# Optimization experiments

Measured on AMD Instinct MI355X. Metric: run time of the kernel, lower is better.

The kernel has to match this reference:

```python
import jax, jax.numpy as jnp
import numpy as np

B, T, C, H = 2, 2048, 2048, 16
HS = C // H
EPS = 1e-5


def _ln(x, w, b):
    mu = jnp.mean(x, axis=-1, keepdims=True)
    var = jnp.mean(jnp.square(x - mu), axis=-1, keepdims=True)
    return (x - mu) * jax.lax.rsqrt(var + EPS) * w + b


def setup_inputs() -> dict:
    key = jax.random.key(0)
    ks = jax.random.split(key, 8)
    s = 0.02
    return {
        "x": jax.random.normal(ks[0], (B, T, C), jnp.float32),
        "ln1_w": jnp.ones((C,), jnp.float32),
        "ln1_b": jnp.zeros((C,), jnp.float32),
        "w_qkv": jax.random.normal(ks[1], (C, 3 * C), jnp.float32) * s,
        "b_qkv": jnp.zeros((3 * C,), jnp.float32),
        "w_proj": jax.random.normal(ks[2], (C, C), jnp.float32) * s,
        "b_proj": jnp.zeros((C,), jnp.float32),
        "ln2_w": jnp.ones((C,), jnp.float32),
        "ln2_b": jnp.zeros((C,), jnp.float32),
        "w_fc": jax.random.normal(ks[3], (C, 4 * C), jnp.float32) * s,
        "b_fc": jnp.zeros((4 * C,), jnp.float32),
        "w_fc2": jax.random.normal(ks[4], (4 * C, C), jnp.float32) * s,
        "b_fc2": jnp.zeros((C,), jnp.float32),
    }


def reference(x, ln1_w, ln1_b, w_qkv, b_qkv, w_proj, b_proj,
              ln2_w, ln2_b, w_fc, b_fc, w_fc2, b_fc2):
    # --- attention branch (kv_cache=None -> L=0, burst=False, no padding mask) ---
    h = _ln(x, ln1_w, ln1_b)
    qkv = h @ w_qkv + b_qkv  # (B, T, 3C)
    q, k, v = jnp.split(qkv, 3, axis=-1)
    q = q.reshape(B, T, H, HS).transpose(0, 2, 1, 3)  # (B, H, T, HS)
    k = k.reshape(B, T, H, HS).transpose(0, 2, 1, 3)
    v = v.reshape(B, T, H, HS).transpose(0, 2, 1, 3)
    att = jnp.einsum('bhqd,bhkd->bhqk', q, k) * (1.0 / np.sqrt(HS))
    causal = jnp.tril(jnp.ones((T, T), bool))  # bias[0:T, 0:T]
    att = jnp.where(causal, att, -jnp.inf)
    att = jax.nn.softmax(att, axis=-1)
    y = jnp.einsum('bhqk,bhkd->bhqd', att, v)
    y = y.transpose(0, 2, 1, 3).reshape(B, T, C)
    y = y @ w_proj + b_proj
    x = x + y
    # --- MLP branch ---
    h = _ln(x, ln2_w, ln2_b)
    h = jax.nn.gelu(h @ w_fc + b_fc, approximate=False)
    x = x + (h @ w_fc2 + b_fc2)
    return x
```

## Files before the change

### kernel.cpp

```cpp
#include <hip/hip_runtime.h>
#include <hip/hip_bf16.h>
#include <cstdint>
#include <cstddef>

typedef __attribute__((ext_vector_type(8))) short bf16x8;
typedef __attribute__((ext_vector_type(4))) float f32x4;

#define DEVI __device__ __forceinline__

DEVI unsigned short f2bf(float f) {
  union { float f; unsigned u; } x; x.f = f;
  unsigned r = x.u + 0x7fffu + ((x.u >> 16) & 1u);
  return (unsigned short)(r >> 16);
}

DEVI float exp2fast(float x) {
#if __has_builtin(__builtin_amdgcn_exp2f)
  return __builtin_amdgcn_exp2f(x);
#else
  return exp2f(x);
#endif
}

DEVI void gload_lds16(const void* g, void* l) {
  __builtin_amdgcn_global_load_lds((const __attribute__((address_space(1))) void*)g,
                                   (__attribute__((address_space(3))) void*)l, 16, 0, 0);
}

DEVI f32x4 mfma16(bf16x8 a, bf16x8 b, f32x4 c) {
  return __builtin_amdgcn_mfma_f32_16x16x32_bf16(a, b, c, 0, 0, 0);
}

__global__ __launch_bounds__(256) void transpose_to_bf16(
    const float* __restrict__ w, unsigned short* __restrict__ wt, int K, int N) {
  __shared__ float tile[32][33];
  const int n0 = blockIdx.x * 32, k0 = blockIdx.y * 32;
  const int tx = threadIdx.x, ty = threadIdx.y;
#pragma unroll
  for (int i = 0; i < 4; i++)
    tile[ty + i * 8][tx] = w[(size_t)(k0 + ty + i * 8) * N + n0 + tx];
  __syncthreads();
#pragma unroll
  for (int i = 0; i < 4; i++)
    wt[(size_t)(n0 + ty + i * 8) * K + k0 + tx] = f2bf(tile[tx][ty + i * 8]);
}

__global__ __launch_bounds__(256) void transpose_v(
    const unsigned short* __restrict__ in, unsigned short* __restrict__ out) {
  __shared__ unsigned short tile[32][33];
  const int bh = blockIdx.z;
  const unsigned short* inp = in + (size_t)bh * 2048 * 128;
  unsigned short* op = out + (size_t)bh * 2048 * 128;
  const int t0 = blockIdx.x * 32, d0 = blockIdx.y * 32;
  const int tx = threadIdx.x, ty = threadIdx.y;
#pragma unroll
  for (int i = 0; i < 4; i++)
    tile[ty + i * 8][tx] = inp[(size_t)(t0 + ty + i * 8) * 128 + d0 + tx];
  __syncthreads();
#pragma unroll
  for (int i = 0; i < 4; i++)
    op[(size_t)(d0 + ty + i * 8) * 2048 + t0 + tx] = tile[tx][ty + i * 8];
}

__global__ __launch_bounds__(256) void ln_kernel(
    const float* __restrict__ x, const float* __restrict__ gw,
    const float* __restrict__ gb, unsigned short* __restrict__ out) {
  __shared__ float red[8];
  const int row = blockIdx.x, tid = threadIdx.x;
  const float* xr = x + (size_t)row * 2048;
  f32x4 a = *((const f32x4*)xr + tid * 2);
  f32x4 b = *((const f32x4*)xr + tid * 2 + 1);
  float s = a[0] + a[1] + a[2] + a[3] + b[0] + b[1] + b[2] + b[3];
#pragma unroll
  for (int m = 32; m >= 1; m >>= 1) s += __shfl_xor(s, m, 64);
  if ((tid & 63) == 0) red[tid >> 6] = s;
  __syncthreads();
  const float mu = (red[0] + red[1] + red[2] + red[3]) * (1.f / 2048.f);
  float d[8]; float ss = 0.f;
#pragma unroll
  for (int j = 0; j < 8; j++) {
    float v = ((j < 4) ? a[j] : b[j - 4]) - mu;
    d[j] = v; ss += v * v;
  }
#pragma unroll
  for (int m = 32; m >= 1; m >>= 1) ss += __shfl_xor(ss, m, 64);
  __syncthreads();
  if ((tid & 63) == 0) red[4 + (tid >> 6)] = ss;
  __syncthreads();
  const float var = (red[4] + red[5] + red[6] + red[7]) * (1.f / 2048.f);
  const float rstd = rsqrtf(var + 1e-5f);
  f32x4 w0 = *((const f32x4*)gw + tid * 2), w1 = *((const f32x4*)gw + tid * 2 + 1);
  f32x4 b0 = *((const f32x4*)gb + tid * 2), b1 = *((const f32x4*)gb + tid * 2 + 1);
  union { bf16x8 v; unsigned short u[8]; } o;
#pragma unroll
  for (int j = 0; j < 8; j++) {
    float wv = (j < 4) ? w0[j] : w1[j - 4];
    float bv = (j < 4) ? b0[j] : b1[j - 4];
    o.u[j] = f2bf(d[j] * rstd * wv + bv);
  }
  *(bf16x8*)(out + (size_t)row * 2048 + tid * 8) = o.v;
}

template <int EPI>
DEVI void epilogue_store(float v, int row, int col, int Nn,
                         const float* __restrict__ res, float* __restrict__ outf,
                         unsigned short* __restrict__ outb, unsigned short* __restrict__ oq,
                         unsigned short* __restrict__ ok, unsigned short* __restrict__ ov) {
  if constexpr (EPI == 0) {
    const int which = col >> 11, cc = col & 2047;
    const int hh = cc >> 7, hs = cc & 127;
    const int bb = row >> 11, tt = row & 2047;
    const size_t bh = (size_t)(bb * 16 + hh);
    const unsigned short bits = f2bf(v);
    if (which == 0) oq[(bh * 2048 + tt) * 128 + hs] = bits;
    else if (which == 1) ok[(bh * 2048 + tt) * 128 + hs] = bits;
    else ov[(bh * 2048 + tt) * 128 + hs] = bits;
  } else if constexpr (EPI == 1) {
    const float ge = 0.5f * v * (1.0f + erff(v * 0.70710678118654752f));
    outb[(size_t)row * Nn + col] = f2bf(ge);
  } else {
    outf[(size_t)row * Nn + col] = v + res[(size_t)row * Nn + col];
  }
}

template <int EPI>
__global__ __launch_bounds__(512, 2) void gemm256(
    const unsigned short* __restrict__ A, const unsigned short* __restrict__ Bt,
    const float* __restrict__ bias, const float* __restrict__ res,
    float* __restrict__ outf, unsigned short* __restrict__ outb,
    unsigned short* __restrict__ oq, unsigned short* __restrict__ ok,
    unsigned short* __restrict__ ov, int Nn, int Kk, int nbn) {
  __shared__ unsigned short As[2][256 * 64];
  __shared__ unsigned short Bs[2][256 * 64];
  const int tid = threadIdx.x;
  const int lane = tid & 63, wid = tid >> 6;
  const int i = lane & 15, g = lane >> 4;
  const int wm = wid >> 2, wn = wid & 3;
  const int nwg = gridDim.x;
  const int sid = (blockIdx.x & 7) * (nwg >> 3) + (blockIdx.x >> 3);
  const int m0 = (sid / nbn) * 256, n0 = (sid % nbn) * 256;

  auto stageA = [&](int bf, int kt, int h) {
#pragma unroll
    for (int c = 0; c < 2; c++) {
      const int cb = h * 1024 + c * 512 + wid * 64;
      const int ci = cb + lane;
      const int row = ci >> 3;
      const int kc = (ci & 7) ^ (row & 7);
      gload_lds16(A + (size_t)(m0 + row) * Kk + kt + kc * 8, &As[bf][(size_t)cb * 8]);
    }
  };
  auto stageB = [&](int bf, int kt, int h) {
#pragma unroll
    for (int c = 0; c < 2; c++) {
      const int cb = h * 1024 + c * 512 + wid * 64;
      const int ci = cb + lane;
      const int row = ci >> 3;
      const int kc = (ci & 7) ^ (row & 7);
      gload_lds16(Bt + (size_t)(n0 + row) * Kk + kt + kc * 8, &Bs[bf][(size_t)cb * 8]);
    }
  };
  auto ldA = [&](int bf, int jj, int ks) -> bf16x8 {
    const int row = (2 * jj + wm) * 16 + i;
    return *(const bf16x8*)((const char*)&As[bf][0] + row * 128 + ((((ks << 2) + g) ^ (i & 7)) << 4));
  };
  auto ldB = [&](int bf, int n, int ks) -> bf16x8 {
    const int row = (4 * n + wn) * 16 + i;
    return *(const bf16x8*)((const char*)&Bs[bf][0] + row * 128 + ((((ks << 2) + g) ^ (i & 7)) << 4));
  };

  f32x4 acc[8][4] = {};
  const int NT = Kk >> 6;

  stageA(0, 0, 0);
  stageB(0, 0, 0);
  stageB(0, 0, 1);
  stageA(0, 0, 1);
  asm volatile("s_waitcnt vmcnt(4)" ::: "memory");
  __builtin_amdgcn_s_barrier();
  __builtin_amdgcn_sched_barrier(0);

  bf16x8 a_lo[4][2], a_hi[4][2], b_lo[2][2], b_hi[2][2];
  for (int t = 0; t < NT; ++t) {
    const int cur = t & 1, nxt = cur ^ 1;
    const int ktn = (t + 1) << 6;
    const bool hn = (t + 1) < NT;
#pragma unroll
    for (int jj = 0; jj < 4; jj++) { a_lo[jj][0] = ldA(cur, jj, 0); a_lo[jj][1] = ldA(cur, jj, 1); }
#pragma unroll
    for (int n = 0; n < 2; n++) { b_lo[n][0] = ldB(cur, n, 0); b_lo[n][1] = ldB(cur, n, 1); }
    if (hn) stageA(nxt, ktn, 0);
    if (hn) asm volatile("s_waitcnt vmcnt(4)" ::: "memory");
    else    asm volatile("s_waitcnt vmcnt(2)" ::: "memory");
    __builtin_amdgcn_s_barrier();
    asm volatile("s_waitcnt lgkmcnt(0)" ::: "memory");
    __builtin_amdgcn_sched_barrier(0);
    __builtin_amdgcn_s_setprio(1);
#pragma unroll
    for (int jj = 0; jj < 4; jj++)
#pragma unroll
      for (int n = 0; n < 2; n++) {
        acc[jj][n] = mfma16(a_lo[jj][0], b_lo[n][0], acc[jj][n]);
        acc[jj][n] = mfma16(a_lo[jj][1], b_lo[n][1], acc[jj][n]);
      }
    __builtin_amdgcn_s_setprio(0);
    __builtin_amdgcn_s_barrier();
    __builtin_amdgcn_sched_barrier(0);
#pragma unroll
    for (int n = 0; n < 2; n++) { b_hi[n][0] = ldB(cur, 2 + n, 0); b_hi[n][1] = ldB(cur, 2 + n, 1); }
    if (hn) stageB(nxt, ktn, 0);
    if (hn) asm volatile("s_waitcnt vmcnt(4)" ::: "memory");
    else    asm volatile("s_waitcnt vmcnt(0)" ::: "memory");
    __builtin_amdgcn_s_barrier();
    asm volatile("s_waitcnt lgkmcnt(0)" ::: "memory");
    __builtin_amdgcn_sched_barrier(0);
    __builtin_amdgcn_s_setprio(1);
#pragma unroll
    for (int jj = 0; jj < 4; jj++)
#pragma unroll
      for (int n = 0; n < 2; n++) {
        acc[jj][2 + n] = mfma16(a_lo[jj][0], b_hi[n][0], acc[jj][2 + n]);
        acc[jj][2 + n] = mfma16(a_lo[jj][1], b_hi[n][1], acc[jj][2 + n]);
      }
    __builtin_amdgcn_s_setprio(0);
    __builtin_amdgcn_s_barrier();
    __builtin_amdgcn_sched_barrier(0);
#pragma unroll
    for (int jj = 0; jj < 4; jj++) { a_hi[jj][0] = ldA(cur, 4 + jj, 0); a_hi[jj][1] = ldA(cur, 4 + jj, 1); }
    if (hn) stageB(nxt, ktn, 1);
    __builtin_amdgcn_s_barrier();
    asm volatile("s_waitcnt lgkmcnt(0)" ::: "memory");
    __builtin_amdgcn_sched_barrier(0);
    __builtin_amdgcn_s_setprio(1);
#pragma unroll
    for (int jj = 0; jj < 4; jj++)
#pragma unroll
      for (int n = 0; n < 2; n++) {
        acc[4 + jj][n] = mfma16(a_hi[jj][0], b_lo[n][0], acc[4 + jj][n]);
        acc[4 + jj][n] = mfma16(a_hi[jj][1], b_lo[n][1], acc[4 + jj][n]);
      }
    __builtin_amdgcn_s_setprio(0);
    __builtin_amdgcn_s_barrier();
    __builtin_amdgcn_sched_barrier(0);
    if (hn) stageA(nxt, ktn, 1);
    if (hn) asm volatile("s_waitcnt vmcnt(4)" ::: "memory");
    __builtin_amdgcn_s_barrier();
    asm volatile("s_waitcnt lgkmcnt(0)" ::: "memory");
    __builtin_amdgcn_sched_barrier(0);
    __builtin_amdgcn_s_setprio(1);
#pragma unroll
    for (int jj = 0; jj < 4; jj++)
#pragma unroll
      for (int n = 0; n < 2; n++) {
        acc[4 + jj][2 + n] = mfma16(a_hi[jj][0], b_hi[n][0], acc[4 + jj][2 + n]);
        acc[4 + jj][2 + n] = mfma16(a_hi[jj][1], b_hi[n][1], acc[4 + jj][2 + n]);
      }
    __builtin_amdgcn_s_setprio(0);
    __builtin_amdgcn_s_barrier();
    __builtin_amdgcn_sched_barrier(0);
  }

#pragma unroll
  for (int jj = 0; jj < 8; jj++)
#pragma unroll
    for (int n = 0; n < 4; n++) {
      const int col = n0 + (4 * n + wn) * 16 + i;
      const float bv = bias[col];
#pragma unroll
      for (int r = 0; r < 4; r++) {
        const int row = m0 + (2 * jj + wm) * 16 + g * 4 + r;
        epilogue_store<EPI>(acc[jj][n][r] + bv, row, col, Nn, res, outf, outb, oq, ok, ov);
      }
    }
}

template <int EPI>
__global__ __launch_bounds__(512, 2) void gemm128(
    const unsigned short* __restrict__ A, const unsigned short* __restrict__ Bt,
    const float* __restrict__ bias, const float* __restrict__ res,
    float* __restrict__ outf, unsigned short* __restrict__ outb,
    unsigned short* __restrict__ oq, unsigned short* __restrict__ ok,
    unsigned short* __restrict__ ov, int Nn, int Kk, int nbn) {
  __shared__ unsigned short As[2][128 * 64];
  __shared__ unsigned short Bs[2][256 * 64];
  const int tid = threadIdx.x;
  const int lane = tid & 63, wid = tid >> 6;
  const int i = lane & 15, g = lane >> 4;
  const int wm = wid >> 2, wn = wid & 3;
  const int nwg = gridDim.x;
  const int sid = (blockIdx.x & 7) * (nwg >> 3) + (blockIdx.x >> 3);
  const int m0 = (sid / nbn) * 128, n0 = (sid % nbn) * 256;

  auto stageA = [&](int bf, int kt) {
#pragma unroll
    for (int c = 0; c < 2; c++) {
      const int cb = c * 512 + wid * 64;
      const int ci = cb + lane;
      const int row = ci >> 3;
      const int kc = (ci & 7) ^ (row & 7);
      gload_lds16(A + (size_t)(m0 + row) * Kk + kt + kc * 8, &As[bf][(size_t)cb * 8]);
    }
  };
  auto stageB = [&](int bf, int kt, int h) {
#pragma unroll
    for (int c = 0; c < 2; c++) {
      const int cb = h * 1024 + c * 512 + wid * 64;
      const int ci = cb + lane;
      const int row = ci >> 3;
      const int kc = (ci & 7) ^ (row & 7);
      gload_lds16(Bt + (size_t)(n0 + row) * Kk + kt + kc * 8, &Bs[bf][(size_t)cb * 8]);
    }
  };
  auto ldA = [&](int bf, int jj, int ks) -> bf16x8 {
    const int row = (2 * jj + wm) * 16 + i;
    return *(const bf16x8*)((const char*)&As[bf][0] + row * 128 + ((((ks << 2) + g) ^ (i & 7)) << 4));
  };
  auto ldB = [&](int bf, int n, int ks) -> bf16x8 {
    const int row = (4 * n + wn) * 16 + i;
    return *(const bf16x8*)((const char*)&Bs[bf][0] + row * 128 + ((((ks << 2) + g) ^ (i & 7)) << 4));
  };

  f32x4 acc[4][4] = {};
  const int NT = Kk >> 6;

  stageA(0, 0);
  stageB(0, 0, 0);
  stageB(0, 0, 1);
  asm volatile("s_waitcnt vmcnt(2)" ::: "memory");
  __builtin_amdgcn_s_barrier();
  __builtin_amdgcn_sched_barrier(0);

  bf16x8 af[4][2], b_lo[2][2], b_hi[2][2];
  for (int t = 0; t < NT; ++t) {
    const int cur = t & 1, nxt = cur ^ 1;
    const int ktn = (t + 1) << 6;
    const bool hn = (t + 1) < NT;
#pragma unroll
    for (int jj = 0; jj < 4; jj++) { af[jj][0] = ldA(cur, jj, 0); af[jj][1] = ldA(cur, jj, 1); }
#pragma unroll
    for (int n = 0; n < 2; n++) { b_lo[n][0] = ldB(cur, n, 0); b_lo[n][1] = ldB(cur, n, 1); }
    if (hn) { stageA(nxt, ktn); stageB(nxt, ktn, 0); stageB(nxt, ktn, 1); }
    if (hn) asm volatile("s_waitcnt vmcnt(6)" ::: "memory");
    else    asm volatile("s_waitcnt vmcnt(0)" ::: "memory");
    __builtin_amdgcn_s_barrier();
    asm volatile("s_waitcnt lgkmcnt(0)" ::: "memory");
    __builtin_amdgcn_sched_barrier(0);
    __builtin_amdgcn_s_setprio(1);
#pragma unroll
    for (int jj = 0; jj < 4; jj++)
#pragma unroll
      for (int n = 0; n < 2; n++) {
        acc[jj][n] = mfma16(af[jj][0], b_lo[n][0], acc[jj][n]);
        acc[jj][n] = mfma16(af[jj][1], b_lo[n][1], acc[jj][n]);
      }
    __builtin_amdgcn_s_setprio(0);
    __builtin_amdgcn_s_barrier();
    __builtin_amdgcn_sched_barrier(0);
#pragma unroll
    for (int n = 0; n < 2; n++) { b_hi[n][0] = ldB(cur, 2 + n, 0); b_hi[n][1] = ldB(cur, 2 + n, 1); }
    if (hn) asm volatile("s_waitcnt vmcnt(2)" ::: "memory");
    else    asm volatile("s_waitcnt vmcnt(0)" ::: "memory");
    __builtin_amdgcn_s_barrier();
    asm volatile("s_waitcnt lgkmcnt(0)" ::: "memory");
    __builtin_amdgcn_sched_barrier(0);
    __builtin_amdgcn_s_setprio(1);
#pragma unroll
    for (int jj = 0; jj < 4; jj++)
#pragma unroll
      for (int n = 0; n < 2; n++) {
        acc[jj][2 + n] = mfma16(af[jj][0], b_hi[n][0], acc[jj][2 + n]);
        acc[jj][2 + n] = mfma16(af[jj][1], b_hi[n][1], acc[jj][2 + n]);
      }
    __builtin_amdgcn_s_setprio(0);
    __builtin_amdgcn_s_barrier();
    __builtin_amdgcn_sched_barrier(0);
  }

#pragma unroll
  for (int jj = 0; jj < 4; jj++)
#pragma unroll
    for (int n = 0; n < 4; n++) {
      const int col = n0 + (4 * n + wn) * 16 + i;
      const float bv = bias[col];
#pragma unroll
      for (int r = 0; r < 4; r++) {
        const int row = m0 + (2 * jj + wm) * 16 + g * 4 + r;
        epilogue_store<EPI>(acc[jj][n][r] + bv, row, col, Nn, res, outf, outb, oq, ok, ov);
      }
    }
}

__global__ __launch_bounds__(256) void attn_kernel(
    const unsigned short* __restrict__ q, const unsigned short* __restrict__ k,
    const unsigned short* __restrict__ vt, unsigned short* __restrict__ y) {
  __shared__ unsigned short Ks[64 * 128];
  __shared__ unsigned short Vs[128 * 64];
  __shared__ unsigned short Ps[4][16 * 64];
  const int tid = threadIdx.x, lane = tid & 63, w = tid >> 6;
  const int i = lane & 15, g = lane >> 4;
  const int p = blockIdx.x, bh = blockIdx.y;
  const int q0A = p * 64, q0B = (31 - p) * 64;
  const int tB = 31 - p;
  const size_t hb = (size_t)bh * (2048 * 128);
  const float sc2 = 0.08838834764831845f * 1.44269504088896341f;

  bf16x8 qfA[4], qfB[4];
  {
    const int qra = q0A + w * 16 + i, qrb = q0B + w * 16 + i;
#pragma unroll
    for (int kc = 0; kc < 4; kc++) {
      qfA[kc] = *(const bf16x8*)(q + hb + (size_t)qra * 128 + kc * 32 + g * 8);
      qfB[kc] = *(const bf16x8*)(q + hb + (size_t)qrb * 128 + kc * 32 + g * 8);
    }
  }
  f32x4 oA[8] = {}, oB[8] = {};
  float mA = -__builtin_inff(), lA = 0.f, mB = -__builtin_inff(), lB = 0.f;

  auto proc = [&](const bf16x8 (&qf)[4], f32x4 (&oacc)[8], float& mrun, float& lrun,
                  bool diag) {
    f32x4 st[4];
#pragma unroll
    for (int ct = 0; ct < 4; ct++) {
      f32x4 a = {};
      const int kvr = ct * 16 + i;
#pragma unroll
      for (int kc = 0; kc < 4; kc++) {
        bf16x8 kf = *(const bf16x8*)((char*)Ks + kvr * 256 + (((kc * 4 + g) ^ (i & 7)) << 4));
        a = mfma16(kf, qf[kc], a);
      }
      st[ct] = a;
    }
    float tm = -__builtin_inff();
    const int ql = w * 16 + i;
#pragma unroll
    for (int ct = 0; ct < 4; ct++)
#pragma unroll
      for (int r = 0; r < 4; r++) {
        float v = st[ct][r] * sc2;
        if (diag) {
          const int kvl = ct * 16 + g * 4 + r;
          if (kvl > ql) v = -__builtin_inff();
        }
        st[ct][r] = v;
        tm = fmaxf(tm, v);
      }
    tm = fmaxf(tm, __shfl_xor(tm, 16, 64));
    tm = fmaxf(tm, __shfl_xor(tm, 32, 64));
    if (!__all(tm - mrun <= 8.f)) {
      const float mnew = fmaxf(mrun, tm);
      const float al = exp2fast(mrun - mnew);
      float ar[4];
#pragma unroll
      for (int r = 0; r < 4; r++) ar[r] = __shfl(al, g * 4 + r, 64);
#pragma unroll
      for (int dt = 0; dt < 8; dt++)
#pragma unroll
        for (int r = 0; r < 4; r++) oacc[dt][r] *= ar[r];
      lrun *= al;
      mrun = mnew;
    }
    float ps = 0.f;
#pragma unroll
    for (int ct = 0; ct < 4; ct++)
#pragma unroll
      for (int r = 0; r < 4; r++) {
        const float pv = exp2fast(st[ct][r] - mrun);
        st[ct][r] = pv;
        ps += pv;
      }
    ps += __shfl_xor(ps, 16, 64);
    ps += __shfl_xor(ps, 32, 64);
    lrun += ps;
#pragma unroll
    for (int ct = 0; ct < 4; ct++) {
      unsigned w0, w1;
      asm("v_cvt_pk_bf16_f32 %0, %1, %2" : "=v"(w0) : "v"(st[ct][0]), "v"(st[ct][1]));
      asm("v_cvt_pk_bf16_f32 %0, %1, %2" : "=v"(w1) : "v"(st[ct][2]), "v"(st[ct][3]));
      char* pb = (char*)&Ps[w][0] + i * 128 +
                 ((((2 * ct + (g >> 1)) ^ (i & 7)) << 4) + (g & 1) * 8);
      *(uint2*)pb = make_uint2(w0, w1);
    }
    bf16x8 pf[2];
#pragma unroll
    for (int kvc = 0; kvc < 2; kvc++)
      pf[kvc] = *(const bf16x8*)((char*)&Ps[w][0] + i * 128 + (((kvc * 4 + g) ^ (i & 7)) << 4));
#pragma unroll
    for (int dt = 0; dt < 8; dt++) {
      const int dr = dt * 16 + i;
#pragma unroll
      for (int kvc = 0; kvc < 2; kvc++) {
        bf16x8 vf = *(const bf16x8*)((char*)Vs + dr * 128 + (((kvc * 4 + g) ^ (dr & 7)) << 4));
        oacc[dt] = mfma16(pf[kvc], vf, oacc[dt]);
      }
    }
  };

  for (int t = 0; t <= tB; ++t) {
    const int j0 = t * 64;
    __syncthreads();
#pragma unroll
    for (int it = 0; it < 4; it++) {
      const int ci = it * 256 + tid;
      const int kv = ci >> 4, ccl = ci & 15;
      gload_lds16(k + hb + (size_t)(j0 + kv) * 128 + ((ccl ^ (kv & 7)) << 3),
                  (char*)Ks + (size_t)(it * 256 + w * 64) * 16);
      const int dd = ci >> 3, c2l = ci & 7;
      gload_lds16(vt + hb + (size_t)dd * 2048 + j0 + ((c2l ^ (dd & 7)) << 3),
                  (char*)Vs + (size_t)(it * 256 + w * 64) * 16);
    }
    __syncthreads();
    if (t <= p) proc(qfA, oA, mA, lA, t == p);
    proc(qfB, oB, mB, lB, t == tB);
  }

  const int bb = bh >> 4, hh = bh & 15;
  auto finish = [&](const f32x4 (&oacc)[8], float lrun, int q0s) {
    const float inv_i = 1.f / lrun;
    float ir[4];
#pragma unroll
    for (int r = 0; r < 4; r++) ir[r] = __shfl(inv_i, g * 4 + r, 64);
#pragma unroll
    for (int r = 0; r < 4; r++) {
      const int row = q0s + w * 16 + g * 4 + r;
#pragma unroll
      for (int dt = 0; dt < 8; dt++) {
        const int d = dt * 16 + i;
        y[((size_t)(bb * 2048 + row)) * 2048 + hh * 128 + d] = f2bf(oacc[dt][r] * ir[r]);
      }
    }
  };
  finish(oA, lA, q0A);
  finish(oB, lB, q0B);
}

extern "C" void kernel_launch(void* const* d_in, const int* in_sizes, int n_in,
                              void* d_out, int out_size, void* d_ws, size_t ws_size,
                              hipStream_t stream) {
  const float* x      = (const float*)d_in[0];
  const float* ln1_w  = (const float*)d_in[1];
  const float* ln1_b  = (const float*)d_in[2];
  const float* w_qkv  = (const float*)d_in[3];
  const float* b_qkv  = (const float*)d_in[4];
  const float* w_proj = (const float*)d_in[5];
  const float* b_proj = (const float*)d_in[6];
  const float* ln2_w  = (const float*)d_in[7];
  const float* ln2_b  = (const float*)d_in[8];
  const float* w_fc   = (const float*)d_in[9];
  const float* b_fc   = (const float*)d_in[10];
  const float* w_fc2  = (const float*)d_in[11];
  const float* b_fc2  = (const float*)d_in[12];

  char* ws = (char*)d_ws;
  unsigned short* wt_qkv  = (unsigned short*)(ws + 0);
  unsigned short* wt_proj = (unsigned short*)(ws + 25165824);
  unsigned short* qb      = (unsigned short*)(ws + 33554432);
  unsigned short* kb      = (unsigned short*)(ws + 50331648);
  unsigned short* wt_fc   = (unsigned short*)(ws + 67108864);
  unsigned short* wt_fc2  = (unsigned short*)(ws + 100663296);
  unsigned short* hb      = (unsigned short*)(ws + 134217728);
  unsigned short* vtb     = (unsigned short*)(ws + 150994944);
  unsigned short* yb      = (unsigned short*)(ws + 167772160);
  float*          x1      = (float*)(ws + 184549376);
  unsigned short* hfc     = (unsigned short*)(ws + 0);
  float* outp = (float*)d_out;

  dim3 tb(32, 8);
  transpose_to_bf16<<<dim3(6144 / 32, 2048 / 32), tb, 0, stream>>>(w_qkv, wt_qkv, 2048, 6144);
  transpose_to_bf16<<<dim3(2048 / 32, 2048 / 32), tb, 0, stream>>>(w_proj, wt_proj, 2048, 2048);
  transpose_to_bf16<<<dim3(8192 / 32, 2048 / 32), tb, 0, stream>>>(w_fc, wt_fc, 2048, 8192);
  transpose_to_bf16<<<dim3(2048 / 32, 8192 / 32), tb, 0, stream>>>(w_fc2, wt_fc2, 8192, 2048);

  ln_kernel<<<4096, 256, 0, stream>>>(x, ln1_w, ln1_b, hb);

  gemm128<0><<<768, 512, 0, stream>>>(
      hb, wt_qkv, b_qkv, nullptr, nullptr, nullptr, qb, kb, yb, 6144, 2048, 24);
  transpose_v<<<dim3(2048 / 32, 128 / 32, 32), tb, 0, stream>>>(yb, vtb);

  attn_kernel<<<dim3(16, 32), 256, 0, stream>>>(qb, kb, vtb, yb);

  gemm128<2><<<256, 512, 0, stream>>>(
      yb, wt_proj, b_proj, x, x1, nullptr, nullptr, nullptr, nullptr, 2048, 2048, 8);

  ln_kernel<<<4096, 256, 0, stream>>>(x1, ln2_w, ln2_b, hb);

  gemm256<1><<<512, 512, 0, stream>>>(
      hb, wt_fc, b_fc, nullptr, nullptr, hfc, nullptr, nullptr, nullptr, 8192, 2048, 32);

  gemm128<2><<<256, 512, 0, stream>>>(
      hfc, wt_fc2, b_fc2, x1, outp, nullptr, nullptr, nullptr, nullptr, 2048, 8192, 8);
}
```

Before: 725.5 us.

## Software-pipeline LDS fragment reads under MFMA phases in both GEMM kernels

Restructures the K-loop of the 256 and 128 tile GEMMs so each phase's LDS fragment reads for the next phase (and the next K tile's first fragments) are issued inside the preceding MFMA block. sched_group_barrier directives interleave MFMA and DS-read groups. The final iteration is peeled so the loop has no runtime has-next branches. This aims to hide LDS read latency behind matrix math, at the cost of more live fragment registers and more complex waitcnt and barrier ordering.

```diff
diff --git a/kernel.cpp b/kernel.cpp
--- a/kernel.cpp
+++ b/kernel.cpp
@@ -123,6 +123,9 @@
   }
 }
 
+#define SGB_MFMA 0x008
+#define SGB_DSRD 0x100
+
 template <int EPI>
 __global__ __launch_bounds__(512, 2) void gemm256(
     const unsigned short* __restrict__ A, const unsigned short* __restrict__ Bt,
@@ -181,83 +184,184 @@
   __builtin_amdgcn_sched_barrier(0);
 
   bf16x8 a_lo[4][2], a_hi[4][2], b_lo[2][2], b_hi[2][2];
-  for (int t = 0; t < NT; ++t) {
+#pragma unroll
+  for (int jj = 0; jj < 4; jj++) { a_lo[jj][0] = ldA(0, jj, 0); a_lo[jj][1] = ldA(0, jj, 1); }
+#pragma unroll
+  for (int n = 0; n < 2; n++) { b_lo[n][0] = ldB(0, n, 0); b_lo[n][1] = ldB(0, n, 1); }
+
+  for (int t = 0; t < NT - 1; ++t) {
     const int cur = t & 1, nxt = cur ^ 1;
     const int ktn = (t + 1) << 6;
-    const bool hn = (t + 1) < NT;
-#pragma unroll
-    for (int jj = 0; jj < 4; jj++) { a_lo[jj][0] = ldA(cur, jj, 0); a_lo[jj][1] = ldA(cur, jj, 1); }
-#pragma unroll
-    for (int n = 0; n < 2; n++) { b_lo[n][0] = ldB(cur, n, 0); b_lo[n][1] = ldB(cur, n, 1); }
-    if (hn) stageA(nxt, ktn, 0);
-    if (hn) asm volatile("s_waitcnt vmcnt(4)" ::: "memory");
-    else    asm volatile("s_waitcnt vmcnt(2)" ::: "memory");
-    __builtin_amdgcn_s_barrier();
-    asm volatile("s_waitcnt lgkmcnt(0)" ::: "memory");
-    __builtin_amdgcn_sched_barrier(0);
-    __builtin_amdgcn_s_setprio(1);
-#pragma unroll
-    for (int jj = 0; jj < 4; jj++)
-#pragma unroll
-      for (int n = 0; n < 2; n++) {
-        acc[jj][n] = mfma16(a_lo[jj][0], b_lo[n][0], acc[jj][n]);
-        acc[jj][n] = mfma16(a_lo[jj][1], b_lo[n][1], acc[jj][n]);
-      }
-    __builtin_amdgcn_s_setprio(0);
-    __builtin_amdgcn_s_barrier();
-    __builtin_amdgcn_sched_barrier(0);
+    stageA(nxt, ktn, 0);
+    asm volatile("s_waitcnt vmcnt(4)" ::: "memory");
+    __builtin_amdgcn_s_barrier();
+    asm volatile("s_waitcnt lgkmcnt(0)" ::: "memory");
+    __builtin_amdgcn_sched_barrier(0);
+    __builtin_amdgcn_s_setprio(1);
+#pragma unroll
+    for (int jj = 0; jj < 4; jj++)
+#pragma unroll
+      for (int n = 0; n < 2; n++) acc[jj][n] = mfma16(a_lo[jj][0], b_lo[n][0], acc[jj][n]);
+#pragma unroll
+    for (int jj = 0; jj < 4; jj++)
+#pragma unroll
+      for (int n = 0; n < 2; n++) acc[jj][n] = mfma16(a_lo[jj][1], b_lo[n][1], acc[jj][n]);
 #pragma unroll
     for (int n = 0; n < 2; n++) { b_hi[n][0] = ldB(cur, 2 + n, 0); b_hi[n][1] = ldB(cur, 2 + n, 1); }
-    if (hn) stageB(nxt, ktn, 0);
-    if (hn) asm volatile("s_waitcnt vmcnt(4)" ::: "memory");
-    else    asm volatile("s_waitcnt vmcnt(0)" ::: "memory");
-    __builtin_amdgcn_s_barrier();
-    asm volatile("s_waitcnt lgkmcnt(0)" ::: "memory");
-    __builtin_amdgcn_sched_barrier(0);
-    __builtin_amdgcn_s_setprio(1);
-#pragma unroll
-    for (int jj = 0; jj < 4; jj++)
-#pragma unroll
-      for (int n = 0; n < 2; n++) {
-        acc[jj][2 + n] = mfma16(a_lo[jj][0], b_hi[n][0], acc[jj][2 + n]);
-        acc[jj][2 + n] = mfma16(a_lo[jj][1], b_hi[n][1], acc[jj][2 + n]);
-      }
-    __builtin_amdgcn_s_setprio(0);
-    __builtin_amdgcn_s_barrier();
-    __builtin_amdgcn_sched_barrier(0);
+#pragma unroll
+    for (int z = 0; z < 4; z++) {
+      __builtin_amdgcn_sched_group_barrier(SGB_MFMA, 4, 0);
+      __builtin_amdgcn_sched_group_barrier(SGB_DSRD, 1, 0);
+    }
+    __builtin_amdgcn_s_setprio(0);
+    __builtin_amdgcn_s_barrier();
+    __builtin_amdgcn_sched_barrier(0);
+    stageB(nxt, ktn, 0);
+    asm volatile("s_waitcnt vmcnt(4)" ::: "memory");
+    __builtin_amdgcn_s_barrier();
+    asm volatile("s_waitcnt lgkmcnt(0)" ::: "memory");
+    __builtin_amdgcn_sched_barrier(0);
+    __builtin_amdgcn_s_setprio(1);
+#pragma unroll
+    for (int jj = 0; jj < 4; jj++)
+#pragma unroll
+      for (int n = 0; n < 2; n++) acc[jj][2 + n] = mfma16(a_lo[jj][0], b_hi[n][0], acc[jj][2 + n]);
+#pragma unroll
+    for (int jj = 0; jj < 4; jj++)
+#pragma unroll
+      for (int n = 0; n < 2; n++) acc[jj][2 + n] = mfma16(a_lo[jj][1], b_hi[n][1], acc[jj][2 + n]);
 #pragma unroll
     for (int jj = 0; jj < 4; jj++) { a_hi[jj][0] = ldA(cur, 4 + jj, 0); a_hi[jj][1] = ldA(cur, 4 + jj, 1); }
-    if (hn) stageB(nxt, ktn, 1);
-    __builtin_amdgcn_s_barrier();
-    asm volatile("s_waitcnt lgkmcnt(0)" ::: "memory");
-    __builtin_amdgcn_sched_barrier(0);
-    __builtin_amdgcn_s_setprio(1);
-#pragma unroll
-    for (int jj = 0; jj < 4; jj++)
-#pragma unroll
-      for (int n = 0; n < 2; n++) {
-        acc[4 + jj][n] = mfma16(a_hi[jj][0], b_lo[n][0], acc[4 + jj][n]);
-        acc[4 + jj][n] = mfma16(a_hi[jj][1], b_lo[n][1], acc[4 + jj][n]);
-      }
-    __builtin_amdgcn_s_setprio(0);
-    __builtin_amdgcn_s_barrier();
-    __builtin_amdgcn_sched_barrier(0);
-    if (hn) stageA(nxt, ktn, 1);
-    if (hn) asm volatile("s_waitcnt vmcnt(4)" ::: "memory");
-    __builtin_amdgcn_s_barrier();
-    asm volatile("s_waitcnt lgkmcnt(0)" ::: "memory");
-    __builtin_amdgcn_sched_barrier(0);
-    __builtin_amdgcn_s_setprio(1);
-#pragma unroll
-    for (int jj = 0; jj < 4; jj++)
-#pragma unroll
-      for (int n = 0; n < 2; n++) {
-        acc[4 + jj][2 + n] = mfma16(a_hi[jj][0], b_hi[n][0], acc[4 + jj][2 + n]);
-        acc[4 + jj][2 + n] = mfma16(a_hi[jj][1], b_hi[n][1], acc[4 + jj][2 + n]);
-      }
-    __builtin_amdgcn_s_setprio(0);
-    __builtin_amdgcn_s_barrier();
-    __builtin_amdgcn_sched_barrier(0);
+#pragma unroll
+    for (int z = 0; z < 8; z++) {
+      __builtin_amdgcn_sched_group_barrier(SGB_MFMA, 2, 0);
+      __builtin_amdgcn_sched_group_barrier(SGB_DSRD, 1, 0);
+    }
+    __builtin_amdgcn_s_setprio(0);
+    __builtin_amdgcn_s_barrier();
+    __builtin_amdgcn_sched_barrier(0);
+    stageB(nxt, ktn, 1);
+    __builtin_amdgcn_s_barrier();
+    asm volatile("s_waitcnt lgkmcnt(0)" ::: "memory");
+    __builtin_amdgcn_sched_barrier(0);
+    __builtin_amdgcn_s_setprio(1);
+#pragma unroll
+    for (int jj = 0; jj < 4; jj++)
+#pragma unroll
+      for (int n = 0; n < 2; n++) acc[4 + jj][n] = mfma16(a_hi[jj][0], b_lo[n][0], acc[4 + jj][n]);
+#pragma unroll
+    for (int jj = 0; jj < 4; jj++)
+#pragma unroll
+      for (int n = 0; n < 2; n++) acc[4 + jj][n] = mfma16(a_hi[jj][1], b_lo[n][1], acc[4 + jj][n]);
+    __builtin_amdgcn_s_setprio(0);
+    __builtin_amdgcn_s_barrier();
+    __builtin_amdgcn_sched_barrier(0);
+    stageA(nxt, ktn, 1);
+    asm volatile("s_waitcnt vmcnt(4)" ::: "memory");
+    __builtin_amdgcn_s_barrier();
+    asm volatile("s_waitcnt lgkmcnt(0)" ::: "memory");
+    __builtin_amdgcn_sched_barrier(0);
+    __builtin_amdgcn_s_setprio(1);
+#pragma unroll
+    for (int jj = 0; jj < 4; jj++)
+#pragma unroll
+      for (int n = 0; n < 2; n++) acc[4 + jj][2 + n] = mfma16(a_hi[jj][0], b_hi[n][0], acc[4 + jj][2 + n]);
+#pragma unroll
+    for (int jj = 0; jj < 4; jj++)
+#pragma unroll
+      for (int n = 0; n < 2; n++) acc[4 + jj][2 + n] = mfma16(a_hi[jj][1], b_hi[n][1], acc[4 + jj][2 + n]);
+#pragma unroll
+    for (int jj = 0; jj < 4; jj++) { a_lo[jj][0] = ldA(nxt, jj, 0); a_lo[jj][1] = ldA(nxt, jj, 1); }
+#pragma unroll
+    for (int n = 0; n < 2; n++) { b_lo[n][0] = ldB(nxt, n, 0); b_lo[n][1] = ldB(nxt, n, 1); }
+#pragma unroll
+    for (int z = 0; z < 4; z++) {
+      __builtin_amdgcn_sched_group_barrier(SGB_MFMA, 2, 0);
+      __builtin_amdgcn_sched_group_barrier(SGB_DSRD, 2, 0);
+    }
+#pragma unroll
+    for (int z = 0; z < 4; z++) {
+      __builtin_amdgcn_sched_group_barrier(SGB_MFMA, 2, 0);
+      __builtin_amdgcn_sched_group_barrier(SGB_DSRD, 1, 0);
+    }
+    __builtin_amdgcn_s_setprio(0);
+    __builtin_amdgcn_s_barrier();
+    __builtin_amdgcn_sched_barrier(0);
+  }
+
+  {
+    const int cur = (NT - 1) & 1;
+    asm volatile("s_waitcnt vmcnt(2)" ::: "memory");
+    __builtin_amdgcn_s_barrier();
+    asm volatile("s_waitcnt lgkmcnt(0)" ::: "memory");
+    __builtin_amdgcn_sched_barrier(0);
+    __builtin_amdgcn_s_setprio(1);
+#pragma unroll
+    for (int jj = 0; jj < 4; jj++)
+#pragma unroll
+      for (int n = 0; n < 2; n++) acc[jj][n] = mfma16(a_lo[jj][0], b_lo[n][0], acc[jj][n]);
+#pragma unroll
+    for (int jj = 0; jj < 4; jj++)
+#pragma unroll
+      for (int n = 0; n < 2; n++) acc[jj][n] = mfma16(a_lo[jj][1], b_lo[n][1], acc[jj][n]);
+#pragma unroll
+    for (int n = 0; n < 2; n++) { b_hi[n][0] = ldB(cur, 2 + n, 0); b_hi[n][1] = ldB(cur, 2 + n, 1); }
+#pragma unroll
+    for (int z = 0; z < 4; z++) {
+      __builtin_amdgcn_sched_group_barrier(SGB_MFMA, 4, 0);
+      __builtin_amdgcn_sched_group_barrier(SGB_DSRD, 1, 0);
+    }
+    __builtin_amdgcn_s_setprio(0);
+    __builtin_amdgcn_s_barrier();
+    __builtin_amdgcn_sched_barrier(0);
+    asm volatile("s_waitcnt vmcnt(0)" ::: "memory");
+    __builtin_amdgcn_s_barrier();
+    asm volatile("s_waitcnt lgkmcnt(0)" ::: "memory");
+    __builtin_amdgcn_sched_barrier(0);
+    __builtin_amdgcn_s_setprio(1);
+#pragma unroll
+    for (int jj = 0; jj < 4; jj++)
+#pragma unroll
+      for (int n = 0; n < 2; n++) acc[jj][2 + n] = mfma16(a_lo[jj][0], b_hi[n][0], acc[jj][2 + n]);
+#pragma unroll
+    for (int jj = 0; jj < 4; jj++)
+#pragma unroll
+      for (int n = 0; n < 2; n++) acc[jj][2 + n] = mfma16(a_lo[jj][1], b_hi[n][1], acc[jj][2 + n]);
+#pragma unroll
+    for (int jj = 0; jj < 4; jj++) { a_hi[jj][0] = ldA(cur, 4 + jj, 0); a_hi[jj][1] = ldA(cur, 4 + jj, 1); }
+#pragma unroll
+    for (int z = 0; z < 8; z++) {
+      __builtin_amdgcn_sched_group_barrier(SGB_MFMA, 2, 0);
+      __builtin_amdgcn_sched_group_barrier(SGB_DSRD, 1, 0);
+    }
+    __builtin_amdgcn_s_setprio(0);
+    __builtin_amdgcn_s_barrier();
+    __builtin_amdgcn_sched_barrier(0);
+    __builtin_amdgcn_s_barrier();
+    asm volatile("s_waitcnt lgkmcnt(0)" ::: "memory");
+    __builtin_amdgcn_sched_barrier(0);
+    __builtin_amdgcn_s_setprio(1);
+#pragma unroll
+    for (int jj = 0; jj < 4; jj++)
+#pragma unroll
+      for (int n = 0; n < 2; n++) acc[4 + jj][n] = mfma16(a_hi[jj][0], b_lo[n][0], acc[4 + jj][n]);
+#pragma unroll
+    for (int jj = 0; jj < 4; jj++)
+#pragma unroll
+      for (int n = 0; n < 2; n++) acc[4 + jj][n] = mfma16(a_hi[jj][1], b_lo[n][1], acc[4 + jj][n]);
+    __builtin_amdgcn_s_setprio(0);
+    __builtin_amdgcn_s_barrier();
+    __builtin_amdgcn_sched_barrier(0);
+    __builtin_amdgcn_s_setprio(1);
+#pragma unroll
+    for (int jj = 0; jj < 4; jj++)
+#pragma unroll
+      for (int n = 0; n < 2; n++) acc[4 + jj][2 + n] = mfma16(a_hi[jj][0], b_hi[n][0], acc[4 + jj][2 + n]);
+#pragma unroll
+    for (int jj = 0; jj < 4; jj++)
+#pragma unroll
+      for (int n = 0; n < 2; n++) acc[4 + jj][2 + n] = mfma16(a_hi[jj][1], b_hi[n][1], acc[4 + jj][2 + n]);
+    __builtin_amdgcn_s_setprio(0);
   }
 
 #pragma unroll
@@ -331,49 +435,109 @@
   __builtin_amdgcn_sched_barrier(0);
 
   bf16x8 af[4][2], b_lo[2][2], b_hi[2][2];
-  for (int t = 0; t < NT; ++t) {
+#pragma unroll
+  for (int jj = 0; jj < 4; jj++) { af[jj][0] = ldA(0, jj, 0); af[jj][1] = ldA(0, jj, 1); }
+#pragma unroll
+  for (int n = 0; n < 2; n++) { b_lo[n][0] = ldB(0, n, 0); b_lo[n][1] = ldB(0, n, 1); }
+
+  for (int t = 0; t < NT - 1; ++t) {
     const int cur = t & 1, nxt = cur ^ 1;
     const int ktn = (t + 1) << 6;
-    const bool hn = (t + 1) < NT;
-#pragma unroll
-    for (int jj = 0; jj < 4; jj++) { af[jj][0] = ldA(cur, jj, 0); af[jj][1] = ldA(cur, jj, 1); }
-#pragma unroll
-    for (int n = 0; n < 2; n++) { b_lo[n][0] = ldB(cur, n, 0); b_lo[n][1] = ldB(cur, n, 1); }
-    if (hn) { stageA(nxt, ktn); stageB(nxt, ktn, 0); stageB(nxt, ktn, 1); }
-    if (hn) asm volatile("s_waitcnt vmcnt(6)" ::: "memory");
-    else    asm volatile("s_waitcnt vmcnt(0)" ::: "memory");
-    __builtin_amdgcn_s_barrier();
-    asm volatile("s_waitcnt lgkmcnt(0)" ::: "memory");
-    __builtin_amdgcn_sched_barrier(0);
-    __builtin_amdgcn_s_setprio(1);
-#pragma unroll
-    for (int jj = 0; jj < 4; jj++)
-#pragma unroll
-      for (int n = 0; n < 2; n++) {
-        acc[jj][n] = mfma16(af[jj][0], b_lo[n][0], acc[jj][n]);
-        acc[jj][n] = mfma16(af[jj][1], b_lo[n][1], acc[jj][n]);
-      }
-    __builtin_amdgcn_s_setprio(0);
-    __builtin_amdgcn_s_barrier();
-    __builtin_amdgcn_sched_barrier(0);
+    stageA(nxt, ktn);
+    stageB(nxt, ktn, 0);
+    stageB(nxt, ktn, 1);
+    asm volatile("s_waitcnt vmcnt(6)" ::: "memory");
+    __builtin_amdgcn_s_barrier();
+    asm volatile("s_waitcnt lgkmcnt(0)" ::: "memory");
+    __builtin_amdgcn_sched_barrier(0);
+    __builtin_amdgcn_s_setprio(1);
+#pragma unroll
+    for (int jj = 0; jj < 4; jj++)
+#pragma unroll
+      for (int n = 0; n < 2; n++) acc[jj][n] = mfma16(af[jj][0], b_lo[n][0], acc[jj][n]);
+#pragma unroll
+    for (int jj = 0; jj < 4; jj++)
+#pragma unroll
+      for (int n = 0; n < 2; n++) acc[jj][n] = mfma16(af[jj][1], b_lo[n][1], acc[jj][n]);
 #pragma unroll
     for (int n = 0; n < 2; n++) { b_hi[n][0] = ldB(cur, 2 + n, 0); b_hi[n][1] = ldB(cur, 2 + n, 1); }
-    if (hn) asm volatile("s_waitcnt vmcnt(2)" ::: "memory");
-    else    asm volatile("s_waitcnt vmcnt(0)" ::: "memory");
-    __builtin_amdgcn_s_barrier();
-    asm volatile("s_waitcnt lgkmcnt(0)" ::: "memory");
-    __builtin_amdgcn_sched_barrier(0);
-    __builtin_amdgcn_s_setprio(1);
-#pragma unroll
-    for (int jj = 0; jj < 4; jj++)
-#pragma unroll
-      for (int n = 0; n < 2; n++) {
-        acc[jj][2 + n] = mfma16(af[jj][0], b_hi[n][0], acc[jj][2 + n]);
-        acc[jj][2 + n] = mfma16(af[jj][1], b_hi[n][1], acc[jj][2 + n]);
-      }
-    __builtin_amdgcn_s_setprio(0);
-    __builtin_amdgcn_s_barrier();
-    __builtin_amdgcn_sched_barrier(0);
+#pragma unroll
+    for (int z = 0; z < 4; z++) {
+      __builtin_amdgcn_sched_group_barrier(SGB_MFMA, 4, 0);
+      __builtin_amdgcn_sched_group_barrier(SGB_DSRD, 1, 0);
+    }
+    __builtin_amdgcn_s_setprio(0);
+    __builtin_amdgcn_s_barrier();
+    __builtin_amdgcn_sched_barrier(0);
+    asm volatile("s_waitcnt vmcnt(2)" ::: "memory");
+    __builtin_amdgcn_s_barrier();
+    asm volatile("s_waitcnt lgkmcnt(0)" ::: "memory");
+    __builtin_amdgcn_sched_barrier(0);
+    __builtin_amdgcn_s_setprio(1);
+#pragma unroll
+    for (int jj = 0; jj < 4; jj++)
+#pragma unroll
+      for (int n = 0; n < 2; n++) acc[jj][2 + n] = mfma16(af[jj][0], b_hi[n][0], acc[jj][2 + n]);
+#pragma unroll
+    for (int jj = 0; jj < 4; jj++)
+#pragma unroll
+      for (int n = 0; n < 2; n++) acc[jj][2 + n] = mfma16(af[jj][1], b_hi[n][1], acc[jj][2 + n]);
+#pragma unroll
+    for (int jj = 0; jj < 4; jj++) { af[jj][0] = ldA(nxt, jj, 0); af[jj][1] = ldA(nxt, jj, 1); }
+#pragma unroll
+    for (int n = 0; n < 2; n++) { b_lo[n][0] = ldB(nxt, n, 0); b_lo[n][1] = ldB(nxt, n, 1); }
+#pragma unroll
+    for (int z = 0; z < 4; z++) {
+      __builtin_amdgcn_sched_group_barrier(SGB_MFMA, 2, 0);
+      __builtin_amdgcn_sched_group_barrier(SGB_DSRD, 2, 0);
+    }
+#pragma unroll
+    for (int z = 0; z < 4; z++) {
+      __builtin_amdgcn_sched_group_barrier(SGB_MFMA, 2, 0);
+      __builtin_amdgcn_sched_group_barrier(SGB_DSRD, 1, 0);
+    }
+    __builtin_amdgcn_s_setprio(0);
+    __builtin_amdgcn_s_barrier();
+    __builtin_amdgcn_sched_barrier(0);
+  }
+
+  {
+    const int cur = (NT - 1) & 1;
+    asm volatile("s_waitcnt vmcnt(0)" ::: "memory");
+    __builtin_amdgcn_s_barrier();
+    asm volatile("s_waitcnt lgkmcnt(0)" ::: "memory");
+    __builtin_amdgcn_sched_barrier(0);
+    __builtin_amdgcn_s_setprio(1);
+#pragma unroll
+    for (int jj = 0; jj < 4; jj++)
+#pragma unroll
+      for (int n = 0; n < 2; n++) acc[jj][n] = mfma16(af[jj][0], b_lo[n][0], acc[jj][n]);
+#pragma unroll
+    for (int jj = 0; jj < 4; jj++)
+#pragma unroll
+      for (int n = 0; n < 2; n++) acc[jj][n] = mfma16(af[jj][1], b_lo[n][1], acc[jj][n]);
+#pragma unroll
+    for (int n = 0; n < 2; n++) { b_hi[n][0] = ldB(cur, 2 + n, 0); b_hi[n][1] = ldB(cur, 2 + n, 1); }
+#pragma unroll
+    for (int z = 0; z < 4; z++) {
+      __builtin_amdgcn_sched_group_barrier(SGB_MFMA, 4, 0);
+      __builtin_amdgcn_sched_group_barrier(SGB_DSRD, 1, 0);
+    }
+    __builtin_amdgcn_s_setprio(0);
+    __builtin_amdgcn_s_barrier();
+    __builtin_amdgcn_sched_barrier(0);
+    asm volatile("s_waitcnt lgkmcnt(0)" ::: "memory");
+    __builtin_amdgcn_sched_barrier(0);
+    __builtin_amdgcn_s_setprio(1);
+#pragma unroll
+    for (int jj = 0; jj < 4; jj++)
+#pragma unroll
+      for (int n = 0; n < 2; n++) acc[jj][2 + n] = mfma16(af[jj][0], b_hi[n][0], acc[jj][2 + n]);
+#pragma unroll
+    for (int jj = 0; jj < 4; jj++)
+#pragma unroll
+      for (int n = 0; n < 2; n++) acc[jj][2 + n] = mfma16(af[jj][1], b_hi[n][1], acc[jj][2 + n]);
+    __builtin_amdgcn_s_setprio(0);
   }
 
 #pragma unroll
```

Result: no change. 728.4 us (+0.4%).
